# Performance work log

Hardware: AMD Instinct MI355X
Metric: run time of the kernel (lower is better)

Reference implementation:

```python
import jax, jax.numpy as jnp
import numpy as np

N_NODES = 50000

def cheb_conv(x, edge_index, W, b):
    # PyG ChebConv, K=2, normalization='sym', lambda_max=2.0 (default):
    # scaled Laplacian L_hat = (2/lambda_max)*L - I = -D^{-1/2} A D^{-1/2} (zero diag).
    # Tx_0 = x, Tx_1 = L_hat @ x ; out = Tx_0 @ W[0] + Tx_1 @ W[1] + b
    src, dst = edge_index[0], edge_index[1]
    ones = jnp.ones(src.shape[0], x.dtype)
    deg = jax.ops.segment_sum(ones, src, num_segments=N_NODES)
    dinv = jnp.where(deg > 0, 1.0 / jnp.sqrt(deg), 0.0)
    norm = -dinv[src] * dinv[dst]                                   # [E]
    tx1 = jax.ops.segment_sum(x[src] * norm[:, None], dst, num_segments=N_NODES)
    return x @ W[0] + tx1 @ W[1] + b

def setup_inputs() -> dict:
    key = jax.random.key(0)
    ks = jax.random.split(key, 12)
    IN, OUT, E, P = 128, 2, 800000, 400000
    return {
        "x": jax.random.normal(ks[0], (N_NODES, IN), jnp.float32),
        "edge_index": jax.random.randint(ks[1], (2, E), 0, N_NODES),
        "E_pos": jax.random.randint(ks[2], (2, P), 0, N_NODES),
        "neg_edge_index": jax.random.randint(ks[3], (2, P), 0, N_NODES),
        "W1": jax.random.normal(ks[4], (2, IN, 300), jnp.float32) * 0.05,
        "b1": jnp.zeros((300,), jnp.float32),
        "W2": jax.random.normal(ks[5], (2, 300, 100), jnp.float32) * 0.05,
        "b2": jnp.zeros((100,), jnp.float32),
        "W3": jax.random.normal(ks[6], (2, 100, OUT), jnp.float32) * 0.05,
        "b3": jnp.zeros((OUT,), jnp.float32),
        "lin1_W": jax.random.normal(ks[7], (100, IN), jnp.float32) * 0.05,
        "lin1_b": jnp.zeros((100,), jnp.float32),
        "lin2_W": jax.random.normal(ks[8], (100, IN), jnp.float32) * 0.05,
        "lin2_b": jnp.zeros((100,), jnp.float32),
        "c1": jnp.full((1,), 0.5, jnp.float32),
        "c2": jnp.full((1,), 0.5, jnp.float32),
    }

def reference(x, edge_index, E_pos, neg_edge_index, W1, b1, W2, b2, W3, b3,
              lin1_W, lin1_b, lin2_W, lin2_b, c1, c2):
    # eval mode: F.dropout and dropout_edge are identity
    x0 = x
    h = jax.nn.relu(cheb_conv(x0, edge_index, W1, b1))
    x1 = jax.nn.relu(cheb_conv(h, edge_index, W2, b2))
    x2 = x1 + jax.nn.relu(x0 @ lin1_W.T + lin1_b)
    z = x1 + jax.nn.relu(x0 @ lin2_W.T + lin2_b)
    pos_score = jnp.sum(z[E_pos[0]] * z[E_pos[1]], axis=1)              # [P]
    pos_loss = -jnp.mean(jnp.log(jax.nn.sigmoid(pos_score) + 1e-15))
    neg_score = jnp.sum(z[neg_edge_index[0]] * z[neg_edge_index[1]], axis=1)
    neg_loss = -jnp.mean(jnp.log(1.0 - jax.nn.sigmoid(neg_score) + 1e-15))
    r_loss = pos_loss + neg_loss
    out = cheb_conv(x2, edge_index, W3, b3)                             # [N, out_channels]
    return (out, r_loss, c1, c2)
```

## Files before the change

### kernel.cpp

```cpp
#include <hip/hip_runtime.h>
#include <math.h>


typedef unsigned short ushort_t;
typedef unsigned char u8;
typedef __attribute__((ext_vector_type(8))) __bf16 bf16x8;
typedef __attribute__((ext_vector_type(8))) short s16x8;
typedef __attribute__((ext_vector_type(4))) float f32x4;
typedef __attribute__((ext_vector_type(2))) float f32x2;

#define NB_H 256
#define HW 12500
#define PW 25000
#define LOSS_NB 1792
#define CAPB 131072

__device__ __forceinline__ f32x4 mfma16x16x32(s16x8 a, s16x8 b, f32x4 c) {
  return __builtin_amdgcn_mfma_f32_16x16x32_bf16(
      __builtin_bit_cast(bf16x8, a), __builtin_bit_cast(bf16x8, b), c, 0, 0, 0);
}
__device__ __forceinline__ ushort_t f2bf(float f) {
  union { float f; unsigned u; } c; c.f = f;
  unsigned r = (c.u + 0x7FFFu + ((c.u >> 16) & 1u)) >> 16;
  return (ushort_t)r;
}
__device__ __forceinline__ f32x2 cvt2lo(unsigned u) {
  return __builtin_amdgcn_cvt_pk_f32_fp8((int)u, false);
}
__device__ __forceinline__ f32x2 cvt2hi(unsigned u) {
  return __builtin_amdgcn_cvt_pk_f32_fp8((int)u, true);
}
__device__ __forceinline__ u8 f2fp8(float f) {
  return (u8)(__builtin_amdgcn_cvt_pk_fp8_f32(f, 0.f, 0, false) & 0xff);
}

template<int VAR, int NT, int KTOT>
__global__ __launch_bounds__(256) void gemm_mfma(
    const ushort_t* __restrict__ A0, const ushort_t* __restrict__ A1,
    const ushort_t* __restrict__ Wt,
    const float* __restrict__ bias0, const float* __restrict__ bias1,
    const float* __restrict__ x1,
    const float* __restrict__ W3c, const float* __restrict__ b3c,
    void* __restrict__ out0, void* __restrict__ out1,
    float* __restrict__ t0g, float* __restrict__ t1g, int M)
{
  constexpr int NF = NT / 32;
  __shared__ __align__(16) ushort_t As[64 * 40];
  __shared__ __align__(16) ushort_t Bs[NT * 40];
  __shared__ float w3s[400];
  const int tid  = threadIdx.x;
  const int lane = tid & 63, w = tid >> 6;
  const int m0 = blockIdx.x * 64;
  const int wm = (w & 1) * 32, wn = (w >> 1) * (NT / 2);
  if (VAR == 2) { for (int i = tid; i < 400; i += 256) w3s[i] = W3c[i]; }
  f32x4 acc[2][NF];
#pragma unroll
  for (int i = 0; i < 2; ++i)
#pragma unroll
    for (int j = 0; j < NF; ++j) acc[i][j] = (f32x4){0.f, 0.f, 0.f, 0.f};

  for (int k0 = 0; k0 < KTOT; k0 += 32) {
    {
      const int r = tid >> 2, c8 = (tid & 3) * 8;
      const int gm = m0 + r;
      uint4 v = {0u, 0u, 0u, 0u};
      if (gm < M) {
        if (VAR == 1) {
          const u8* s8 = (const u8*)A0 + (size_t)gm * 320 + k0 + c8;
          const uint2 r8 = *(const uint2*)s8;
          const f32x2 f0 = cvt2lo(r8.x), f1 = cvt2hi(r8.x);
          const f32x2 f2 = cvt2lo(r8.y), f3 = cvt2hi(r8.y);
          v.x = (unsigned)f2bf(f0.x) | ((unsigned)f2bf(f0.y) << 16);
          v.y = (unsigned)f2bf(f1.x) | ((unsigned)f2bf(f1.y) << 16);
          v.z = (unsigned)f2bf(f2.x) | ((unsigned)f2bf(f2.y) << 16);
          v.w = (unsigned)f2bf(f3.x) | ((unsigned)f2bf(f3.y) << 16);
        } else {
          const ushort_t* srcp;
          if (VAR == 0) srcp = (k0 < 128) ? A0 + (size_t)gm * 128 + k0 + c8
                                          : A1 + (size_t)gm * 128 + (k0 - 128) + c8;
          else srcp = A0 + (size_t)gm * 128 + k0 + c8;
          v = *(const uint4*)srcp;
        }
      }
      *(uint4*)&As[r * 40 + c8] = v;
    }
    {
      const int c8 = (tid & 3) * 8;
#pragma unroll
      for (int i = 0; i < (NT * 4 + 255) / 256; ++i) {
        const int r = (tid >> 2) + i * 64;
        if (r < NT)
          *(uint4*)&Bs[r * 40 + c8] = *(const uint4*)(Wt + (size_t)r * KTOT + k0 + c8);
      }
    }
    __syncthreads();
    s16x8 af[2], bfr[NF];
#pragma unroll
    for (int mi = 0; mi < 2; ++mi)
      af[mi] = *(const s16x8*)&As[(wm + mi * 16 + (lane & 15)) * 40 + (lane >> 4) * 8];
#pragma unroll
    for (int ni = 0; ni < NF; ++ni)
      bfr[ni] = *(const s16x8*)&Bs[(wn + ni * 16 + (lane & 15)) * 40 + (lane >> 4) * 8];
#pragma unroll
    for (int mi = 0; mi < 2; ++mi)
#pragma unroll
      for (int ni = 0; ni < NF; ++ni)
        acc[mi][ni] = mfma16x16x32(af[mi], bfr[ni], acc[mi][ni]);
    __syncthreads();
  }

  if (VAR == 2) {
#pragma unroll
    for (int mi = 0; mi < 2; ++mi)
#pragma unroll
      for (int r = 0; r < 4; ++r) {
        const int gRow = m0 + wm + mi * 16 + ((lane >> 4) << 2) + r;
        float p0 = 0.f, p1 = 0.f, p2 = 0.f, p3 = 0.f;
#pragma unroll
        for (int ni = 0; ni < NF; ++ni) {
          const int col = wn + ni * 16 + (lane & 15);
          const float v = acc[mi][ni][r];
          if (gRow < M) {
            if (col < 100) {
              const float x2v = x1[(size_t)gRow * 128 + col] + fmaxf(v + bias0[col], 0.f);
              p0 = fmaf(x2v, w3s[col * 2 + 0], p0);
              p1 = fmaf(x2v, w3s[col * 2 + 1], p1);
              p2 = fmaf(x2v, w3s[200 + col * 2 + 0], p2);
              p3 = fmaf(x2v, w3s[200 + col * 2 + 1], p3);
            } else if (col < 200) {
              const int c = col - 100;
              ((u8*)out1)[(size_t)gRow * 128 + c] =
                  f2fp8(x1[(size_t)gRow * 128 + c] + fmaxf(v + bias1[c], 0.f));
            }
          }
        }
        if (wn == 0) {
#pragma unroll
          for (int off = 8; off; off >>= 1) {
            p0 += __shfl_down(p0, off, 16);
            p1 += __shfl_down(p1, off, 16);
            p2 += __shfl_down(p2, off, 16);
            p3 += __shfl_down(p3, off, 16);
          }
          if ((lane & 15) == 0 && gRow < M) {
            t0g[(size_t)gRow * 2 + 0] = p0 + b3c[0];
            t0g[(size_t)gRow * 2 + 1] = p1 + b3c[1];
            t1g[(size_t)gRow * 2 + 0] = p2;
            t1g[(size_t)gRow * 2 + 1] = p3;
          }
        }
      }
  } else {
#pragma unroll
    for (int mi = 0; mi < 2; ++mi)
#pragma unroll
      for (int ni = 0; ni < NF; ++ni)
#pragma unroll
        for (int r = 0; r < 4; ++r) {
          const int gRow = m0 + wm + mi * 16 + ((lane >> 4) << 2) + r;
          const int col  = wn + ni * 16 + (lane & 15);
          if (gRow >= M) continue;
          const float v = acc[mi][ni][r];
          if (VAR == 0) {
            ((u8*)out0)[(size_t)gRow * 320 + col] =
                (col < 300) ? f2fp8(fmaxf(v + bias0[col], 0.f)) : (u8)0;
          } else {
            if (col < 100) ((float*)out0)[(size_t)gRow * 128 + col] = v + bias0[col];
            else if (col < 200) ((u8*)out1)[(size_t)gRow * 128 + (col - 100)] = f2fp8(v);
          }
        }
  }
}

__global__ __launch_bounds__(256) void prep(
    const int* __restrict__ src, const int* __restrict__ dst, int E, int M,
    unsigned* __restrict__ partS, unsigned* __restrict__ partD,
    ushort_t* __restrict__ rank,
    const float* __restrict__ x, ushort_t* __restrict__ xb,
    u8* __restrict__ xf8, int n4,
    const float* __restrict__ W1, const float* __restrict__ W2,
    const float* __restrict__ l1W, const float* __restrict__ l2W,
    ushort_t* __restrict__ W1t, ushort_t* __restrict__ W2t,
    ushort_t* __restrict__ Wlt,
    const int* __restrict__ ep, const int* __restrict__ en, int P,
    int sd, int nbkt, unsigned* __restrict__ bCnt, int2* __restrict__ plist)
{
  __shared__ unsigned hist[HW];
  const int blk = blockIdx.x;
  if (blk < 512) {
    const int isD = (blk >= 256);
    const int b = isD ? blk - 256 : blk;
    const int* keys = isD ? dst : src;
    unsigned* part = isD ? partD : partS;
    const int cs = (E + NB_H - 1) / NB_H;
    const int e0 = b * cs;
    const int e1 = (e0 + cs < E) ? e0 + cs : E;
    for (int r = 0; r < 2; ++r) {
      const int klo = r * 2 * HW;
      for (int i = threadIdx.x; i < HW; i += 256) hist[i] = 0;
      __syncthreads();
      for (int e = e0 + threadIdx.x; e < e1; e += 256) {
        const int k = keys[e] - klo;
        if ((unsigned)k < (unsigned)(2 * HW)) {
          const unsigned old = atomicAdd(&hist[k >> 1], (k & 1) ? 0x10000u : 1u);
          if (isD) rank[e] = (ushort_t)((old >> ((k & 1) * 16)) & 0xffffu);
        }
      }
      __syncthreads();
      for (int i = threadIdx.x; i < HW; i += 256)
        part[(size_t)b * PW + r * HW + i] = hist[i];
      __syncthreads();
    }
    return;
  }
  if (blk < 512 + nbkt) {
    __shared__ unsigned lcnt[8], lbase[8];
    const int t = threadIdx.x;
    if (t < 8) lcnt[t] = 0u;
    __syncthreads();
    const int i = (blk - 512) * 256 + t;
    const int valid = (i < 2 * P);
    int bkt = 0; unsigned rnk = 0; int2 rec = make_int2(0, 0);
    if (valid) {
      const int neg = (i >= P);
      const int p = neg ? i - P : i;
      const int* ia = neg ? en : ep;
      const int na = ia[p], nb = ia[P + p];
      bkt = na / sd;
      rec.x = na;
      rec.y = (int)((unsigned)nb | (neg ? 0x80000000u : 0u));
      rnk = atomicAdd(&lcnt[bkt], 1u);
    }
    __syncthreads();
    if (t < 8) lbase[t] = lcnt[t] ? atomicAdd(&bCnt[t], lcnt[t]) : 0u;
    __syncthreads();
    if (valid) {
      const unsigned pos = lbase[bkt] + rnk;
      if (pos < (unsigned)CAPB)
        plist[(size_t)bkt * CAPB + pos] = rec;
    }
    return;
  }
  const int i = (blk - 512 - nbkt) * 256 + threadIdx.x;
  if (i < n4) {
    const float4 v = ((const float4*)x)[i];
    ushort4 o; o.x = f2bf(v.x); o.y = f2bf(v.y); o.z = f2bf(v.z); o.w = f2bf(v.w);
    ((ushort4*)xb)[i] = o;
    int p = 0;
    p = __builtin_amdgcn_cvt_pk_fp8_f32(v.x, v.y, p, false);
    p = __builtin_amdgcn_cvt_pk_fp8_f32(v.z, v.w, p, true);
    ((unsigned*)xf8)[i] = (unsigned)p;
    return;
  }
  const int j = i - n4;
  if (j < 81920) {
    const int n = j >> 8, k = j & 255;
    float v = 0.f;
    if (n < 300) v = (k < 128) ? W1[k * 300 + n] : W1[38400 + (k - 128) * 300 + n];
    W1t[j] = f2bf(v);
  } else if (j < 153600) {
    const int jj = j - 81920;
    const int n = jj / 320, k = jj - n * 320;
    float v = 0.f;
    if (n < 200 && k < 300) v = W2[(n < 100 ? 0 : 30000) + k * 100 + (n % 100)];
    W2t[jj] = f2bf(v);
  } else if (j < 182272) {
    const int jj = j - 153600;
    const int n = jj >> 7, k = jj & 127;
    float v = 0.f;
    if (n < 100) v = l1W[n * 128 + k];
    else if (n < 200) v = l2W[(n - 100) * 128 + k];
    Wlt[jj] = f2bf(v);
  }
}

__global__ __launch_bounds__(256) void reduce_base2(
    const unsigned* __restrict__ partS, unsigned* __restrict__ partD,
    float* __restrict__ dinv, int* __restrict__ cnt, int M)
{
  const int t = blockIdx.x * 256 + threadIdx.x;
  if (t < PW) {
    const int i = t;
    unsigned ssum = 0;
    for (int b = 0; b < NB_H; b += 8) {
      unsigned v[8];
#pragma unroll
      for (int q = 0; q < 8; ++q) v[q] = partS[(size_t)(b + q) * PW + i];
#pragma unroll
      for (int q = 0; q < 8; ++q) ssum += v[q];
    }
    const int k = 2 * i;
    const unsigned s0 = ssum & 0xffffu, s1 = ssum >> 16;
    if (k < M) dinv[k] = s0 ? 1.f / sqrtf((float)s0) : 0.f;
    if (k + 1 < M) dinv[k + 1] = s1 ? 1.f / sqrtf((float)s1) : 0.f;
  } else if (t < 2 * PW) {
    const int i = t - PW;
    unsigned run = 0;
    for (int b = 0; b < NB_H; b += 8) {
      unsigned v[8], pre[8];
#pragma unroll
      for (int q = 0; q < 8; ++q) v[q] = partD[(size_t)(b + q) * PW + i];
#pragma unroll
      for (int q = 0; q < 8; ++q) { pre[q] = run; run += v[q]; }
#pragma unroll
      for (int q = 0; q < 8; ++q) partD[(size_t)(b + q) * PW + i] = pre[q];
    }
    const int k = 2 * i;
    if (k < M) cnt[k] = (int)(run & 0xffffu);
    if (k + 1 < M) cnt[k + 1] = (int)(run >> 16);
  }
}

__global__ void scan_local(const int* __restrict__ cnt, int* __restrict__ ptr,
                           int* __restrict__ bsum, int n)
{
  __shared__ int tmp[256];
  const int i = blockIdx.x * 256 + threadIdx.x;
  const int v = (i < n) ? cnt[i] : 0;
  tmp[threadIdx.x] = v;
  __syncthreads();
  for (int off = 1; off < 256; off <<= 1) {
    const int t = (threadIdx.x >= off) ? tmp[threadIdx.x - off] : 0;
    __syncthreads();
    tmp[threadIdx.x] += t;
    __syncthreads();
  }
  if (i < n) ptr[i] = tmp[threadIdx.x] - v;
  if (threadIdx.x == 255) bsum[blockIdx.x] = tmp[255];
}
__global__ void scan_add2(int* __restrict__ ptr, const int* __restrict__ bsum,
                          int n, int E, int nb, float* __restrict__ accs)
{
  __shared__ int tmp[256];
  const int v = (threadIdx.x < nb) ? bsum[threadIdx.x] : 0;
  tmp[threadIdx.x] = v;
  __syncthreads();
  for (int off = 1; off < 256; off <<= 1) {
    const int t = (threadIdx.x >= off) ? tmp[threadIdx.x - off] : 0;
    __syncthreads();
    tmp[threadIdx.x] += t;
    __syncthreads();
  }
  __syncthreads();
  const int offset = (blockIdx.x > 0) ? tmp[blockIdx.x - 1] : 0;
  const int i = blockIdx.x * 256 + threadIdx.x;
  if (i < n) ptr[i] += offset;
  if (i == 0) { ptr[n] = E; accs[0] = 0.f; accs[1] = 0.f; }
}

__global__ void fill_csr2(const int* __restrict__ src, const int* __restrict__ dst,
                          const float* __restrict__ dinv, const int* __restrict__ ptr,
                          const unsigned* __restrict__ base32,
                          const ushort_t* __restrict__ rank,
                          int2* __restrict__ csr, int E)
{
  const int e = blockIdx.x * 256 + threadIdx.x;
  if (e >= E) return;
  const int cs = (E + NB_H - 1) / NB_H;
  const int b = e / cs;
  const int s = src[e], d = dst[e];
  const unsigned bv = base32[(size_t)b * PW + (d >> 1)];
  const int base = (int)((bv >> ((d & 1) * 16)) & 0xffffu);
  const int pos = ptr[d] + base + (int)rank[e];
  const float w = -dinv[s] * dinv[d];
  csr[pos] = make_int2(s, __float_as_int(w));
}

#define ACCV(u, ww) { f32x2 t; \
  t = cvt2lo(u.x); a[0]  = fmaf(ww, t.x, a[0]);  a[1]  = fmaf(ww, t.y, a[1]);  \
  t = cvt2hi(u.x); a[2]  = fmaf(ww, t.x, a[2]);  a[3]  = fmaf(ww, t.y, a[3]);  \
  t = cvt2lo(u.y); a[4]  = fmaf(ww, t.x, a[4]);  a[5]  = fmaf(ww, t.y, a[5]);  \
  t = cvt2hi(u.y); a[6]  = fmaf(ww, t.x, a[6]);  a[7]  = fmaf(ww, t.y, a[7]);  \
  t = cvt2lo(u.z); a[8]  = fmaf(ww, t.x, a[8]);  a[9]  = fmaf(ww, t.y, a[9]);  \
  t = cvt2hi(u.z); a[10] = fmaf(ww, t.x, a[10]); a[11] = fmaf(ww, t.y, a[11]); \
  t = cvt2lo(u.w); a[12] = fmaf(ww, t.x, a[12]); a[13] = fmaf(ww, t.y, a[13]); \
  t = cvt2hi(u.w); a[14] = fmaf(ww, t.x, a[14]); a[15] = fmaf(ww, t.y, a[15]); }

__global__ __launch_bounds__(256) void gather128e(
    const u8* __restrict__ xf8, ushort_t* __restrict__ txb,
    const int* __restrict__ ptr, const int2* __restrict__ csr, int M)
{
  const int node = (blockIdx.x * 256 + threadIdx.x) >> 3;
  const int sub  = threadIdx.x & 7;
  if (node >= M) return;
  const int beg = ptr[node], end = ptr[node + 1];
  float a[16] = {};
  int p = beg;
  for (; p + 8 <= end; p += 8) {
    int2 e[8];
#pragma unroll
    for (int q = 0; q < 8; ++q) e[q] = csr[p + q];
    uint4 v[8];
#pragma unroll
    for (int q = 0; q < 8; ++q)
      v[q] = *(const uint4*)(xf8 + (size_t)e[q].x * 128 + sub * 16);
#pragma unroll
    for (int q = 0; q < 8; ++q) { const float wq = __int_as_float(e[q].y); ACCV(v[q], wq) }
  }
  for (; p < end; ++p) {
    const int2 eq = csr[p]; const float wq = __int_as_float(eq.y);
    const uint4 v = *(const uint4*)(xf8 + (size_t)eq.x * 128 + sub * 16);
    ACCV(v, wq)
  }
  uint4 o1, o2;
  o1.x = (unsigned)f2bf(a[0])  | ((unsigned)f2bf(a[1])  << 16);
  o1.y = (unsigned)f2bf(a[2])  | ((unsigned)f2bf(a[3])  << 16);
  o1.z = (unsigned)f2bf(a[4])  | ((unsigned)f2bf(a[5])  << 16);
  o1.w = (unsigned)f2bf(a[6])  | ((unsigned)f2bf(a[7])  << 16);
  o2.x = (unsigned)f2bf(a[8])  | ((unsigned)f2bf(a[9])  << 16);
  o2.y = (unsigned)f2bf(a[10]) | ((unsigned)f2bf(a[11]) << 16);
  o2.z = (unsigned)f2bf(a[12]) | ((unsigned)f2bf(a[13]) << 16);
  o2.w = (unsigned)f2bf(a[14]) | ((unsigned)f2bf(a[15]) << 16);
  ushort_t* dstp = txb + (size_t)node * 128 + sub * 16;
  *(uint4*)dstp = o1;
  *(uint4*)(dstp + 8) = o2;
}

__global__ __launch_bounds__(256) void gather100e_x1(
    const u8* __restrict__ Brh, float* __restrict__ Ar,
    const int* __restrict__ ptr, const int2* __restrict__ csr, int M)
{
  const int node = (blockIdx.x * 256 + threadIdx.x) >> 3;
  const int sub  = threadIdx.x & 7;
  if (node >= M) return;
  const int beg = ptr[node], end = ptr[node + 1];
  float a[16] = {};
  int p = beg;
  for (; p + 8 <= end; p += 8) {
    int2 e[8];
#pragma unroll
    for (int q = 0; q < 8; ++q) e[q] = csr[p + q];
    uint4 v[8];
#pragma unroll
    for (int q = 0; q < 8; ++q)
      v[q] = *(const uint4*)(Brh + (size_t)e[q].x * 128 + sub * 16);
#pragma unroll
    for (int q = 0; q < 8; ++q) { const float wq = __int_as_float(e[q].y); ACCV(v[q], wq) }
  }
  for (; p < end; ++p) {
    const int2 eq = csr[p]; const float wq = __int_as_float(eq.y);
    const uint4 v = *(const uint4*)(Brh + (size_t)eq.x * 128 + sub * 16);
    ACCV(v, wq)
  }
  float* dstp = Ar + (size_t)node * 128 + sub * 16;
#pragma unroll
  for (int q = 0; q < 4; ++q) {
    float4 b = *(const float4*)(dstp + q * 4);
    b.x = fmaxf(b.x + a[q * 4 + 0], 0.f);
    b.y = fmaxf(b.y + a[q * 4 + 1], 0.f);
    b.z = fmaxf(b.z + a[q * 4 + 2], 0.f);
    b.w = fmaxf(b.w + a[q * 4 + 3], 0.f);
    *(float4*)(dstp + q * 4) = b;
  }
}
#undef ACCV

__device__ __forceinline__ void maskrow(uint4& r, int sub) {
  if (sub >= 6) { r.y = 0u; r.z = 0u; r.w = 0u; if (sub == 7) r.x = 0u; }
}
#define DOTV(uu, vv, s) { f32x2 p_, q_; \
  p_ = cvt2lo(uu.x); q_ = cvt2lo(vv.x); s = fmaf(p_.x, q_.x, s); s = fmaf(p_.y, q_.y, s); \
  p_ = cvt2hi(uu.x); q_ = cvt2hi(vv.x); s = fmaf(p_.x, q_.x, s); s = fmaf(p_.y, q_.y, s); \
  p_ = cvt2lo(uu.y); q_ = cvt2lo(vv.y); s = fmaf(p_.x, q_.x, s); s = fmaf(p_.y, q_.y, s); \
  p_ = cvt2hi(uu.y); q_ = cvt2hi(vv.y); s = fmaf(p_.x, q_.x, s); s = fmaf(p_.y, q_.y, s); \
  p_ = cvt2lo(uu.z); q_ = cvt2lo(vv.z); s = fmaf(p_.x, q_.x, s); s = fmaf(p_.y, q_.y, s); \
  p_ = cvt2hi(uu.z); q_ = cvt2hi(vv.z); s = fmaf(p_.x, q_.x, s); s = fmaf(p_.y, q_.y, s); \
  p_ = cvt2lo(uu.w); q_ = cvt2lo(vv.w); s = fmaf(p_.x, q_.x, s); s = fmaf(p_.y, q_.y, s); \
  p_ = cvt2hi(uu.w); q_ = cvt2hi(vv.w); s = fmaf(p_.x, q_.x, s); s = fmaf(p_.y, q_.y, s); }

__global__ __launch_bounds__(256) void loss_g2(
    const u8* __restrict__ zf8, const int2* __restrict__ plist,
    const unsigned* __restrict__ bCnt, float* __restrict__ acc,
    const float* __restrict__ t1, const float* __restrict__ t0,
    const int* __restrict__ ptr, const int2* __restrict__ csr,
    float* __restrict__ out, int M)
{
  const int tid = threadIdx.x;
  if (blockIdx.x >= LOSS_NB) {
    const int i = (blockIdx.x - LOSS_NB) * 256 + tid;
    if (i >= M) return;
    float a0 = 0.f, a1 = 0.f;
    const int beg = ptr[i], end = ptr[i + 1];
    int p = beg;
    for (; p + 4 <= end; p += 4) {
      const int2 e0 = csr[p], e1 = csr[p + 1], e2 = csr[p + 2], e3 = csr[p + 3];
      const float w0 = __int_as_float(e0.y), w1 = __int_as_float(e1.y);
      const float w2 = __int_as_float(e2.y), w3 = __int_as_float(e3.y);
      const float2 v0 = *(const float2*)(t1 + (size_t)e0.x * 2);
      const float2 v1 = *(const float2*)(t1 + (size_t)e1.x * 2);
      const float2 v2 = *(const float2*)(t1 + (size_t)e2.x * 2);
      const float2 v3 = *(const float2*)(t1 + (size_t)e3.x * 2);
      a0 = fmaf(w0, v0.x, a0); a1 = fmaf(w0, v0.y, a1);
      a0 = fmaf(w1, v1.x, a0); a1 = fmaf(w1, v1.y, a1);
      a0 = fmaf(w2, v2.x, a0); a1 = fmaf(w2, v2.y, a1);
      a0 = fmaf(w3, v3.x, a0); a1 = fmaf(w3, v3.y, a1);
    }
    for (; p < end; ++p) {
      const int2 eq = csr[p]; const float wq = __int_as_float(eq.y);
      const float2 v = *(const float2*)(t1 + (size_t)eq.x * 2);
      a0 = fmaf(wq, v.x, a0); a1 = fmaf(wq, v.y, a1);
    }
    const float2 base = *(const float2*)(t0 + (size_t)i * 2);
    *(float2*)(out + (size_t)i * 2) = make_float2(base.x + a0, base.y + a1);
    return;
  }
  __shared__ float red[8];
  const int lane = tid & 63, wib = tid >> 6;
  const int sub = tid & 7;
  const int bkt = blockIdx.x & 7;
  const int wk  = (int)(blockIdx.x >> 3);
  const int slot0 = wk * 32 + (tid >> 3);
  const int step = (LOSS_NB / 8) * 32;
  const int cnt = min((int)bCnt[bkt], CAPB);
  const int2* bl = plist + (size_t)bkt * CAPB;
  float tp = 0.f, tn = 0.f;
  int g = slot0;
  for (; g + 3 * step < cnt; g += 4 * step) {
    int2 pr[4];
#pragma unroll
    for (int q = 0; q < 4; ++q) pr[q] = bl[g + q * step];
    uint4 ra[4], rb[4];
#pragma unroll
    for (int q = 0; q < 4; ++q) {
      const int nbv = pr[q].y & 0x7fffffff;
      rb[q] = *(const uint4*)(zf8 + (size_t)nbv * 128 + sub * 16);
      ra[q] = *(const uint4*)(zf8 + (size_t)pr[q].x * 128 + sub * 16);
      maskrow(ra[q], sub); maskrow(rb[q], sub);
    }
    float s[4] = {0.f, 0.f, 0.f, 0.f};
#pragma unroll
    for (int q = 0; q < 4; ++q) DOTV(ra[q], rb[q], s[q])
#pragma unroll
    for (int off = 4; off; off >>= 1) {
#pragma unroll
      for (int q = 0; q < 4; ++q) s[q] += __shfl_down(s[q], off, 8);
    }
    if (sub == 0) {
#pragma unroll
      for (int q = 0; q < 4; ++q) {
        const float sig = 1.f / (1.f + expf(-s[q]));
        if ((unsigned)pr[q].y >> 31) tn += logf(1.f - sig + 1e-15f);
        else tp += logf(sig + 1e-15f);
      }
    }
  }
  for (; g < cnt; g += step) {
    const int2 pr = bl[g];
    const int nbv = pr.y & 0x7fffffff;
    uint4 rb = *(const uint4*)(zf8 + (size_t)nbv * 128 + sub * 16);
    uint4 ra = *(const uint4*)(zf8 + (size_t)pr.x * 128 + sub * 16);
    maskrow(ra, sub); maskrow(rb, sub);
    float s = 0.f;
    DOTV(ra, rb, s)
#pragma unroll
    for (int off = 4; off; off >>= 1) s += __shfl_down(s, off, 8);
    if (sub == 0) {
      const float sig = 1.f / (1.f + expf(-s));
      if ((unsigned)pr.y >> 31) tn += logf(1.f - sig + 1e-15f);
      else tp += logf(sig + 1e-15f);
    }
  }
  tp += __shfl_down(tp, 32, 64); tn += __shfl_down(tn, 32, 64);
  tp += __shfl_down(tp, 16, 64); tn += __shfl_down(tn, 16, 64);
  tp += __shfl_down(tp, 8, 64);  tn += __shfl_down(tn, 8, 64);
  if (lane == 0) { red[wib] = tp; red[4 + wib] = tn; }
  __syncthreads();
  if (tid == 0) {
    atomicAdd(acc + 0, red[0] + red[1] + red[2] + red[3]);
    atomicAdd(acc + 1, red[4] + red[5] + red[6] + red[7]);
  }
}
#undef DOTV

__global__ void final_scalars(const float* __restrict__ accs,
                              const float* __restrict__ c1, const float* __restrict__ c2,
                              float* __restrict__ out, int M, float invP)
{
  out[2 * M + 0] = -(accs[0] + accs[1]) * invP;
  out[2 * M + 1] = c1[0];
  out[2 * M + 2] = c2[0];
}

extern "C" void kernel_launch(void* const* d_in, const int* in_sizes, int n_in,
                              void* d_out, int out_size, void* d_ws, size_t ws_size,
                              hipStream_t stream)
{
  const float* x   = (const float*)d_in[0];
  const int*   ei  = (const int*)d_in[1];
  const int*   ep  = (const int*)d_in[2];
  const int*   en  = (const int*)d_in[3];
  const float* W1  = (const float*)d_in[4];
  const float* b1  = (const float*)d_in[5];
  const float* W2  = (const float*)d_in[6];
  const float* b2  = (const float*)d_in[7];
  const float* W3  = (const float*)d_in[8];
  const float* b3  = (const float*)d_in[9];
  const float* l1W = (const float*)d_in[10];
  const float* l1b = (const float*)d_in[11];
  const float* l2W = (const float*)d_in[12];
  const float* l2b = (const float*)d_in[13];
  const float* c1  = (const float*)d_in[14];
  const float* c2  = (const float*)d_in[15];
  float* out = (float*)d_out;

  const int M = in_sizes[0] / 128;
  const int E = in_sizes[1] / 2;
  const int P = in_sizes[2] / 2;
  const int* src = ei;
  const int* dst = ei + E;
  const int nb_scan = (M + 255) / 256;
  const int sd = (M + 7) / 8;
  const int nbkt = (2 * P + 255) / 256;

  float* ws = (float*)d_ws;
  size_t o = 0;
  float*    dinv = ws + o;            o += 50176;
  int*      cnt  = (int*)(ws + o);    o += (size_t)M;
  int*      ptr  = (int*)(ws + o);    o += (size_t)M + 8;
  int*      bsum = (int*)(ws + o);    o += 256;
  int2*     csr  = (int2*)(ws + o);   o += (size_t)E * 2;
  ushort_t* rank = (ushort_t*)(ws + o); o += (size_t)E / 2;
  ushort_t* xb   = (ushort_t*)(ws + o); o += (size_t)M * 64;
  u8*       xf8  = (u8*)(ws + o);     o += (size_t)M * 32;
  ushort_t* tx0b = (ushort_t*)(ws + o); o += (size_t)M * 64;
  ushort_t* W1t  = (ushort_t*)(ws + o); o += 40960;
  ushort_t* W2t  = (ushort_t*)(ws + o); o += 35840;
  ushort_t* Wlt  = (ushort_t*)(ws + o); o += 14336;
  u8*       h8   = (u8*)(ws + o);     o += (size_t)M * 160;
  float*    Ar   = ws + o;            o += (size_t)M * 128;
  u8*       Brh  = (u8*)(ws + o);     o += (size_t)M * 32;
  u8*       zf8  = (u8*)(ws + o);     o += (size_t)M * 32;
  float*    t0   = ws + o;            o += (size_t)M * 2;
  float*    t1   = ws + o;            o += (size_t)M * 2;
  float*    accs = ws + o;            o += 8;
  unsigned* bCnt = (unsigned*)(ws + o); o += 16;
  int2*     plist = (int2*)(ws + o);  o += (size_t)8 * CAPB * 2;
  unsigned* partS = (unsigned*)h8;
  unsigned* partD = (unsigned*)Ar;

  hipMemsetAsync(bCnt, 0, 8 * sizeof(unsigned), stream);

  const int n4 = M * 32;
  const int packBlocks = (n4 + 182272 + 255) / 256;
  prep<<<512 + nbkt + packBlocks, 256, 0, stream>>>(
      src, dst, E, M, partS, partD, rank,
      x, xb, xf8, n4, W1, W2, l1W, l2W, W1t, W2t, Wlt,
      ep, en, P, sd, nbkt, bCnt, plist);

  reduce_base2<<<(2 * PW + 255) / 256, 256, 0, stream>>>(partS, partD, dinv, cnt, M);
  scan_local<<<nb_scan, 256, 0, stream>>>(cnt, ptr, bsum, M);
  scan_add2<<<nb_scan, 256, 0, stream>>>(ptr, bsum, M, E, nb_scan, accs);
  fill_csr2<<<(E + 255) / 256, 256, 0, stream>>>(src, dst, dinv, ptr, partD, rank, csr, E);

  const int gB = (M + 63) / 64;
  const int gE8 = (M * 8 + 255) / 256;

  gather128e<<<gE8, 256, 0, stream>>>(xf8, tx0b, ptr, csr, M);
  gemm_mfma<0, 320, 256><<<gB, 256, 0, stream>>>(
      xb, tx0b, W1t, b1, nullptr, nullptr, nullptr, nullptr, h8, nullptr, nullptr, nullptr, M);

  gemm_mfma<1, 224, 320><<<gB, 256, 0, stream>>>(
      (const ushort_t*)h8, nullptr, W2t, b2, nullptr, nullptr, nullptr, nullptr,
      Ar, Brh, nullptr, nullptr, M);
  gather100e_x1<<<gE8, 256, 0, stream>>>(Brh, Ar, ptr, csr, M);

  gemm_mfma<2, 224, 128><<<gB, 256, 0, stream>>>(
      xb, nullptr, Wlt, l1b, l2b, Ar , W3, b3, nullptr, zf8, t0, t1, M);

  loss_g2<<<LOSS_NB + nb_scan, 256, 0, stream>>>(
      zf8, plist, bCnt, accs, t1, t0, ptr, csr, out, M);
  final_scalars<<<1, 1, 0, stream>>>(accs, c1, c2, out, M, 1.0f / (float)P);
}
```

Measured before the change: 478.9 us.

## Bucket loss pairs by both endpoints and fold bucketing into CSR fill

```diff
diff --git a/kernel.cpp b/kernel.cpp
--- a/kernel.cpp
+++ b/kernel.cpp
@@ -14,6 +14,7 @@
 #define PW 25000
 #define LOSS_NB 1792
 #define CAPB 131072
+#define GTBL 0x2375326476015410ULL
 
 __device__ __forceinline__ f32x4 mfma16x16x32(s16x8 a, s16x8 b, f32x4 c) {
   return __builtin_amdgcn_mfma_f32_16x16x32_bf16(
@@ -181,9 +182,7 @@
     const float* __restrict__ W1, const float* __restrict__ W2,
     const float* __restrict__ l1W, const float* __restrict__ l2W,
     ushort_t* __restrict__ W1t, ushort_t* __restrict__ W2t,
-    ushort_t* __restrict__ Wlt,
-    const int* __restrict__ ep, const int* __restrict__ en, int P,
-    int sd, int nbkt, unsigned* __restrict__ bCnt, int2* __restrict__ plist)
+    ushort_t* __restrict__ Wlt)
 {
   __shared__ unsigned hist[HW];
   const int blk = blockIdx.x;
@@ -213,35 +212,7 @@
     }
     return;
   }
-  if (blk < 512 + nbkt) {
-    __shared__ unsigned lcnt[8], lbase[8];
-    const int t = threadIdx.x;
-    if (t < 8) lcnt[t] = 0u;
-    __syncthreads();
-    const int i = (blk - 512) * 256 + t;
-    const int valid = (i < 2 * P);
-    int bkt = 0; unsigned rnk = 0; int2 rec = make_int2(0, 0);
-    if (valid) {
-      const int neg = (i >= P);
-      const int p = neg ? i - P : i;
-      const int* ia = neg ? en : ep;
-      const int na = ia[p], nb = ia[P + p];
-      bkt = na / sd;
-      rec.x = na;
-      rec.y = (int)((unsigned)nb | (neg ? 0x80000000u : 0u));
-      rnk = atomicAdd(&lcnt[bkt], 1u);
-    }
-    __syncthreads();
-    if (t < 8) lbase[t] = lcnt[t] ? atomicAdd(&bCnt[t], lcnt[t]) : 0u;
-    __syncthreads();
-    if (valid) {
-      const unsigned pos = lbase[bkt] + rnk;
-      if (pos < (unsigned)CAPB)
-        plist[(size_t)bkt * CAPB + pos] = rec;
-    }
-    return;
-  }
-  const int i = (blk - 512 - nbkt) * 256 + threadIdx.x;
+  const int i = (blk - 512) * 256 + threadIdx.x;
   if (i < n4) {
     const float4 v = ((const float4*)x)[i];
     ushort4 o; o.x = f2bf(v.x); o.y = f2bf(v.y); o.z = f2bf(v.z); o.w = f2bf(v.w);
@@ -329,7 +300,8 @@
   if (threadIdx.x == 255) bsum[blockIdx.x] = tmp[255];
 }
 __global__ void scan_add2(int* __restrict__ ptr, const int* __restrict__ bsum,
-                          int n, int E, int nb, float* __restrict__ accs)
+                          int n, int E, int nb, float* __restrict__ accs,
+                          unsigned* __restrict__ bCnt)
 {
   __shared__ int tmp[256];
   const int v = (threadIdx.x < nb) ? bsum[threadIdx.x] : 0;
@@ -346,15 +318,48 @@
   const int i = blockIdx.x * 256 + threadIdx.x;
   if (i < n) ptr[i] += offset;
   if (i == 0) { ptr[n] = E; accs[0] = 0.f; accs[1] = 0.f; }
-}
-
-__global__ void fill_csr2(const int* __restrict__ src, const int* __restrict__ dst,
-                          const float* __restrict__ dinv, const int* __restrict__ ptr,
-                          const unsigned* __restrict__ base32,
-                          const ushort_t* __restrict__ rank,
-                          int2* __restrict__ csr, int E)
-{
-  const int e = blockIdx.x * 256 + threadIdx.x;
+  if (blockIdx.x == 0 && threadIdx.x < 8) bCnt[threadIdx.x] = 0u;
+}
+
+__global__ __launch_bounds__(256) void fill_csr2_pb(
+    const int* __restrict__ src, const int* __restrict__ dst,
+    const float* __restrict__ dinv, const int* __restrict__ ptr,
+    const unsigned* __restrict__ base32, const ushort_t* __restrict__ rank,
+    int2* __restrict__ csr, int E, int fillNB,
+    const int* __restrict__ ep, const int* __restrict__ en, int P,
+    int sd, unsigned* __restrict__ bCnt, int2* __restrict__ plist)
+{
+  const int blk = blockIdx.x;
+  if (blk >= fillNB) {
+    __shared__ unsigned lcnt[8], lbase[8];
+    const int t = threadIdx.x;
+    if (t < 8) lcnt[t] = 0u;
+    __syncthreads();
+    const int i = (blk - fillNB) * 256 + t;
+    const int valid = (i < 2 * P);
+    int bkt = 0; unsigned rnk = 0; int2 rec = make_int2(0, 0);
+    if (valid) {
+      const int neg = (i >= P);
+      const int p = neg ? i - P : i;
+      const int* ia = neg ? en : ep;
+      const int na = ia[p], nb = ia[P + p];
+      const int hx = (na / sd) >> 1, hy = (nb / sd) >> 1;
+      bkt = (int)((GTBL >> ((hx * 4 + hy) * 4)) & 7ULL);
+      rec.x = na;
+      rec.y = (int)((unsigned)nb | (neg ? 0x80000000u : 0u));
+      rnk = atomicAdd(&lcnt[bkt], 1u);
+    }
+    __syncthreads();
+    if (t < 8) lbase[t] = lcnt[t] ? atomicAdd(&bCnt[t], lcnt[t]) : 0u;
+    __syncthreads();
+    if (valid) {
+      const unsigned pos = lbase[bkt] + rnk;
+      if (pos < (unsigned)CAPB)
+        plist[(size_t)bkt * CAPB + pos] = rec;
+    }
+    return;
+  }
+  const int e = blk * 256 + threadIdx.x;
   if (e >= E) return;
   const int cs = (E + NB_H - 1) / NB_H;
   const int b = e / cs;
@@ -610,7 +615,8 @@
   const int* dst = ei + E;
   const int nb_scan = (M + 255) / 256;
   const int sd = (M + 7) / 8;
-  const int nbkt = (2 * P + 255) / 256;
+  const int fillNB = (E + 255) / 256;
+  const int pbNB = (2 * P + 255) / 256;
 
   float* ws = (float*)d_ws;
   size_t o = 0;
@@ -638,19 +644,18 @@
   unsigned* partS = (unsigned*)h8;
   unsigned* partD = (unsigned*)Ar;
 
-  hipMemsetAsync(bCnt, 0, 8 * sizeof(unsigned), stream);
-
   const int n4 = M * 32;
   const int packBlocks = (n4 + 182272 + 255) / 256;
-  prep<<<512 + nbkt + packBlocks, 256, 0, stream>>>(
+  prep<<<512 + packBlocks, 256, 0, stream>>>(
       src, dst, E, M, partS, partD, rank,
-      x, xb, xf8, n4, W1, W2, l1W, l2W, W1t, W2t, Wlt,
-      ep, en, P, sd, nbkt, bCnt, plist);
+      x, xb, xf8, n4, W1, W2, l1W, l2W, W1t, W2t, Wlt);
 
   reduce_base2<<<(2 * PW + 255) / 256, 256, 0, stream>>>(partS, partD, dinv, cnt, M);
   scan_local<<<nb_scan, 256, 0, stream>>>(cnt, ptr, bsum, M);
-  scan_add2<<<nb_scan, 256, 0, stream>>>(ptr, bsum, M, E, nb_scan, accs);
-  fill_csr2<<<(E + 255) / 256, 256, 0, stream>>>(src, dst, dinv, ptr, partD, rank, csr, E);
+  scan_add2<<<nb_scan, 256, 0, stream>>>(ptr, bsum, M, E, nb_scan, accs, bCnt);
+  fill_csr2_pb<<<fillNB + pbNB, 256, 0, stream>>>(
+      src, dst, dinv, ptr, partD, rank, csr, E, fillNB,
+      ep, en, P, sd, bCnt, plist);
 
   const int gB = (M + 63) / 64;
   const int gE8 = (M * 8 + 255) / 256;
```

Result: no change. 486.2 us (+1.5%).
